# Optimization experiments

Measured on AMD Instinct MI355X. Metric: run time of the kernel, lower is better.

## Reference

```python
import jax, jax.numpy as jnp
import numpy as np

B = 4096        # batch
N_IN = 4096     # flattened input size
C = 128         # number of cores
A = 64          # axons (inputs) per core
O = 64          # neurons (outputs) per core
N_OUT = 1024    # number of output sources
CYCLES = 4      # ChipLatency
POOL_W = N_IN + 2 + C * O  # x cols | off(zero) | always_on(one) | core buffers


def setup_inputs() -> dict:
    key = jax.random.key(0)
    k1, k2, k3, k4 = jax.random.split(key, 4)
    x = jax.random.normal(k1, (B, N_IN), dtype=jnp.float32)
    # core_params[c] has shape (neurons_out, axons_in) = (O, A)
    W = jax.random.normal(k2, (C, O, A), dtype=jnp.float32) * 0.05
    # flat source index per (core, axon): encodes (is_input / is_off / is_always_on / buffer[core][neuron])
    axon_idx = jax.random.randint(k3, (C, A), 0, POOL_W, dtype=jnp.int32)
    out_idx = jax.random.randint(k4, (N_OUT,), 0, POOL_W, dtype=jnp.int32)
    return {"x": x, "W": W, "axon_idx": axon_idx, "out_idx": out_idx, "cycles": CYCLES}


def reference(x, W, axon_idx, out_idx, cycles):
    b = x.shape[0]
    c, o, a = W.shape
    zero_col = jnp.zeros((b, 1), x.dtype)   # is_off sources
    one_col = jnp.ones((b, 1), x.dtype)     # is_always_on sources
    buffers = jnp.zeros((b, c * o), x.dtype)  # all core buffers, flattened core-major

    def make_pool(buf):
        return jnp.concatenate([x, zero_col, one_col, buf], axis=1)  # (b, POOL_W)

    for _ in range(cycles):
        pool = make_pool(buffers)
        inp = pool[:, axon_idx]  # (b, c, a) fused get_signal_tensor gather
        # buffer[c] = relu(input_signals[c] @ core_matrix[c]) == relu(W[c] @ inp[c].T).T
        buffers = jax.nn.relu(jnp.einsum('coa,bca->bco', W, inp)).reshape(b, c * o)

    pool = make_pool(buffers)
    return pool[:, out_idx]  # (b, N_OUT) output_sources gather
```

## Files before the change

### kernel.cpp

```cpp
#include <hip/hip_runtime.h>

typedef __attribute__((ext_vector_type(8))) short short8;
typedef __attribute__((ext_vector_type(8))) __bf16 bf16x8;
typedef __attribute__((ext_vector_type(4))) float f32x4;
typedef __attribute__((ext_vector_type(4))) unsigned short ushort4_t;
typedef __attribute__((ext_vector_type(4))) unsigned int uint4_t;

#define NB   4096
#define NIN  4096
#define NX   4098
#define NC   128
#define NO   64
#define NA   64
#define NOUT 1024

__device__ __forceinline__ unsigned short f2bf(float f) {
  unsigned b = __builtin_bit_cast(unsigned, f);
  b += 0x7FFFu + ((b >> 16) & 1u);
  return (unsigned short)(b >> 16);
}
__device__ __forceinline__ float bf2f(unsigned short u) {
  return __builtin_bit_cast(float, (unsigned)u << 16);
}

__global__ __launch_bounds__(256) void prep_kernel(
    const float* __restrict__ x, const float* __restrict__ W,
    unsigned short* __restrict__ xT, unsigned short* __restrict__ Wb) {
  int bid = blockIdx.x, t = threadIdx.x;
  if (bid < 4096) {
    __shared__ unsigned short tile[64][68];
    int b0 = (bid >> 6) << 6, n0 = (bid & 63) << 6;
    int r = t >> 4, c4 = (t & 15) << 2;
#pragma unroll
    for (int rr = 0; rr < 4; ++rr) {
      int row = r + rr * 16;
      float4 v = *(const float4*)(x + (size_t)(b0 + row) * NIN + n0 + c4);
      tile[row][c4 + 0] = f2bf(v.x);
      tile[row][c4 + 1] = f2bf(v.y);
      tile[row][c4 + 2] = f2bf(v.z);
      tile[row][c4 + 3] = f2bf(v.w);
    }
    __syncthreads();
#pragma unroll
    for (int rr = 0; rr < 4; ++rr) {
      int nl = r + rr * 16;
      ushort4_t o;
      o.x = tile[c4 + 0][nl];
      o.y = tile[c4 + 1][nl];
      o.z = tile[c4 + 2][nl];
      o.w = tile[c4 + 3][nl];
      *(ushort4_t*)(xT + (size_t)(n0 + nl) * NB + b0 + c4) = o;
    }
  } else if (bid < 4096 + 256) {
    size_t i0 = (size_t)(bid - 4096) * 2048 + (size_t)t * 8;
    float4 v0 = *(const float4*)(W + i0);
    float4 v1 = *(const float4*)(W + i0 + 4);
    ushort4_t a, b;
    a.x = f2bf(v0.x); a.y = f2bf(v0.y); a.z = f2bf(v0.z); a.w = f2bf(v0.w);
    b.x = f2bf(v1.x); b.y = f2bf(v1.y); b.z = f2bf(v1.z); b.w = f2bf(v1.w);
    *(ushort4_t*)(Wb + i0) = a;
    *(ushort4_t*)(Wb + i0 + 4) = b;
  } else {
    int e = (bid - 4352) * 1024 + t * 4;
    int row = e >> 12, col = e & 4095;
    unsigned short val = (row == 0) ? (unsigned short)0 : (unsigned short)0x3F80;
    ushort4_t o = {val, val, val, val};
    *(ushort4_t*)(xT + (size_t)(NIN + row) * NB + col) = o;
  }
}

__global__ __launch_bounds__(1024) void mask_kernel(
    const int* __restrict__ oidx, unsigned char* __restrict__ mask) {
  int t = threadIdx.x;
#pragma unroll
  for (int i = t; i < NC * NO; i += 1024) mask[i] = 0;
  __syncthreads();
  if (t < NOUT) {
    int idx = oidx[t];
    if (idx >= NX) mask[idx - NX] = 1;
  }
}

template <int MODE>
__global__ __launch_bounds__(256) void cycle_kernel(
    const unsigned short* __restrict__ xT, const unsigned short* __restrict__ Wb,
    const unsigned short* __restrict__ bufPrev, unsigned short* __restrict__ bufNext,
    const int* __restrict__ axon, const unsigned char* __restrict__ mask,
    int first) {
  __shared__ __align__(16) unsigned short SM[64 * 264];
  int c = blockIdx.y;
  int t = threadIdx.x;
  int b0 = blockIdx.x << 8;
  const int* arow = axon + (c << 6);

  {
    int ao = t >> 5, bo = t & 31;
    const int* ar = arow + ao * 8;
    uint4_t rows[8];
#pragma unroll
    for (int r = 0; r < 8; ++r) {
      int idx = ar[r];
      const unsigned short* s = nullptr;
      if (idx < NX)      s = xT + (size_t)idx * NB;
      else if (!first)   s = bufPrev + (size_t)(idx - NX) * NB;
      if (s) rows[r] = *(const uint4_t*)(s + b0 + bo * 8);
      else   rows[r] = (uint4_t)(0u);
    }
    unsigned lo[4][4], hi[4][4];
#pragma unroll
    for (int p = 0; p < 4; ++p)
#pragma unroll
      for (int k = 0; k < 4; ++k) {
        unsigned wi = rows[2 * p][k], wj = rows[2 * p + 1][k];
        lo[p][k] = __builtin_amdgcn_perm(wj, wi, 0x05040100u);
        hi[p][k] = __builtin_amdgcn_perm(wj, wi, 0x07060302u);
      }
#pragma unroll
    for (int e = 0; e < 8; ++e) {
      int k = e >> 1;
      uint4_t col;
      if (e & 1) { col[0] = hi[0][k]; col[1] = hi[1][k]; col[2] = hi[2][k]; col[3] = hi[3][k]; }
      else       { col[0] = lo[0][k]; col[1] = lo[1][k]; col[2] = lo[2][k]; col[3] = lo[3][k]; }
      int b = bo * 8 + e;
      int sw = ao ^ (b & 7) ^ ((b >> 5) & 7);
      *(uint4_t*)&SM[b * 64 + (sw << 3)] = col;
    }
  }
  __syncthreads();

  int lane = t & 63, w = t >> 6;
  int ln = lane & 15, g = lane >> 4;
  const unsigned short* wrow = Wb + ((size_t)c << 12);

  f32x4 acc[4][4];
#pragma unroll
  for (int i = 0; i < 4; ++i)
#pragma unroll
    for (int j = 0; j < 4; ++j) acc[i][j] = (f32x4)(0.f);

#pragma unroll
  for (int ks = 0; ks < 2; ++ks) {
    short8 bw[4];
#pragma unroll
    for (int j = 0; j < 4; ++j)
      bw[j] = *(const short8*)(wrow + ((size_t)(j * 16 + ln) << 6) + ks * 32 + g * 8);

    short8 ag[4];
#pragma unroll
    for (int i = 0; i < 4; ++i) {
      int bl = (w << 6) + (i << 4) + ln;
      int c8 = (ks << 2) + g;
      int sw = c8 ^ (bl & 7) ^ ((bl >> 5) & 7);
      ag[i] = *(const short8*)&SM[bl * 64 + (sw << 3)];
    }

#pragma unroll
    for (int i = 0; i < 4; ++i)
#pragma unroll
      for (int j = 0; j < 4; ++j)
        acc[i][j] = __builtin_amdgcn_mfma_f32_16x16x32_bf16(
            __builtin_bit_cast(bf16x8, ag[i]), __builtin_bit_cast(bf16x8, bw[j]),
            acc[i][j], 0, 0, 0);
  }

  __syncthreads();
#pragma unroll
  for (int j = 0; j < 4; ++j) {
    int o = j * 16 + ln;
#pragma unroll
    for (int i = 0; i < 4; ++i) {
      ushort4_t pk;
#pragma unroll
      for (int r = 0; r < 4; ++r) pk[r] = f2bf(fmaxf(acc[i][j][r], 0.f));
      *(ushort4_t*)&SM[o * 264 + (w << 6) + (i << 4) + (g << 2)] = pk;
    }
  }
  __syncthreads();
#pragma unroll
  for (int it = 0; it < 16; ++it) {
    int row = it * 4 + w;
    if (MODE == 1 && mask[(c << 6) + row] == 0) continue;
    ushort4_t v = *(const ushort4_t*)&SM[row * 264 + (lane << 2)];
    *(ushort4_t*)(bufNext + ((size_t)((c << 6) + row)) * NB + b0 + (lane << 2)) = v;
  }
}

__global__ __launch_bounds__(256) void final_kernel(
    const unsigned short* __restrict__ xT, const unsigned short* __restrict__ bufFin,
    const int* __restrict__ out_idx, float* __restrict__ out) {
  __shared__ unsigned short tile[256][66];
  int j0 = blockIdx.x << 6, b0 = blockIdx.y << 8;
  int t = threadIdx.x;
  {
    int jl = t >> 2, bq = t & 3;
    int idx = out_idx[j0 + jl];
    const unsigned short* src = (idx < NX) ? xT + (size_t)idx * NB
                                           : bufFin + (size_t)(idx - NX) * NB;
    int jcol = jl ^ (bq << 4);
#pragma unroll
    for (int k = 0; k < 8; ++k) {
      short8 v = *(const short8*)(src + b0 + bq * 64 + k * 8);
#pragma unroll
      for (int m = 0; m < 8; ++m)
        tile[bq * 64 + k * 8 + m][jcol] = (unsigned short)v[m];
    }
  }
  __syncthreads();
  {
    int j = t & 63, ws = t >> 6;
#pragma unroll
    for (int bb = 0; bb < 64; ++bb) {
      int b = bb * 4 + ws;
      int jc = j ^ ((b >> 6) << 4);
      out[(size_t)(b0 + b) * NOUT + j0 + j] = bf2f(tile[b][jc]);
    }
  }
}

extern "C" void kernel_launch(void* const* d_in, const int* in_sizes, int n_in,
                              void* d_out, int out_size, void* d_ws, size_t ws_size,
                              hipStream_t stream) {
  const float* x    = (const float*)d_in[0];
  const float* W    = (const float*)d_in[1];
  const int*   axon = (const int*)d_in[2];
  const int*   oidx = (const int*)d_in[3];
  float* out = (float*)d_out;

  const size_t XT_BYTES  = (size_t)NX * NB * 2;
  const size_t WB_BYTES  = (size_t)NC * NO * NA * 2;
  const size_t BUF_BYTES = (size_t)NC * NO * NB * 2;
  const size_t MASK_B    = 8192;
  if (ws_size < XT_BYTES + WB_BYTES + 2 * BUF_BYTES + MASK_B) return;

  char* ws = (char*)d_ws;
  unsigned short* xT   = (unsigned short*)ws;
  unsigned short* Wb   = (unsigned short*)(ws + XT_BYTES);
  unsigned short* bufA = (unsigned short*)(ws + XT_BYTES + WB_BYTES);
  unsigned short* bufB = (unsigned short*)(ws + XT_BYTES + WB_BYTES + BUF_BYTES);
  unsigned char*  mask = (unsigned char*)(ws + XT_BYTES + WB_BYTES + 2 * BUF_BYTES);

  prep_kernel<<<4360, 256, 0, stream>>>(x, W, xT, Wb);
  mask_kernel<<<1, 1024, 0, stream>>>(oidx, mask);
  dim3 cg(NB / 256, NC);
  cycle_kernel<0><<<cg, 256, 0, stream>>>(xT, Wb, bufB, bufA, axon, mask, 1);
  cycle_kernel<0><<<cg, 256, 0, stream>>>(xT, Wb, bufA, bufB, axon, mask, 0);
  cycle_kernel<0><<<cg, 256, 0, stream>>>(xT, Wb, bufB, bufA, axon, mask, 0);
  cycle_kernel<1><<<cg, 256, 0, stream>>>(xT, Wb, bufA, bufB, axon, mask, 0);
  final_kernel<<<dim3(NOUT / 64, NB / 256), 256, 0, stream>>>(xT, bufB, oidx, out);
}
```

Measured before the change: 155.8 us.

## Skip buffer writes for unreferenced neurons and widen cycle blocks to 512 batch rows

A second mask is built from the axon indices, so the intermediate cycles only write buffer rows that some later axon actually reads. The output mask is kept for the last cycle. In that last cycle, whole 16-neuron groups with no referenced neuron also skip their weight loads and MFMAs. The cycle kernel now handles 512 batch rows per block with 512 threads and writes 16-byte stores, which halves the grid and doubles the LDS per block. The intent is to cut write bandwidth and wasted matrix work, at the cost of lower occupancy per CU.

```diff
diff --git a/kernel.cpp b/kernel.cpp
--- a/kernel.cpp
+++ b/kernel.cpp
@@ -70,31 +70,38 @@
 }
 
 __global__ __launch_bounds__(1024) void mask_kernel(
-    const int* __restrict__ oidx, unsigned char* __restrict__ mask) {
+    const int* __restrict__ axon, const int* __restrict__ oidx,
+    unsigned char* __restrict__ gmask, unsigned char* __restrict__ omask) {
   int t = threadIdx.x;
-#pragma unroll
-  for (int i = t; i < NC * NO; i += 1024) mask[i] = 0;
-  __syncthreads();
+  for (int i = t; i < NC * NO; i += 1024) { gmask[i] = 0; omask[i] = 0; }
+  __syncthreads();
+  for (int i = t; i < NC * NA; i += 1024) {
+    int idx = axon[i];
+    if (idx >= NX) gmask[idx - NX] = 1;
+  }
   if (t < NOUT) {
     int idx = oidx[t];
-    if (idx >= NX) mask[idx - NX] = 1;
+    if (idx >= NX) omask[idx - NX] = 1;
   }
 }
 
 template <int MODE>
-__global__ __launch_bounds__(256) void cycle_kernel(
+__global__ __launch_bounds__(512) void cycle_kernel(
     const unsigned short* __restrict__ xT, const unsigned short* __restrict__ Wb,
     const unsigned short* __restrict__ bufPrev, unsigned short* __restrict__ bufNext,
     const int* __restrict__ axon, const unsigned char* __restrict__ mask,
     int first) {
-  __shared__ __align__(16) unsigned short SM[64 * 264];
+  __shared__ __align__(16) unsigned short SM[64 * 520];
   int c = blockIdx.y;
   int t = threadIdx.x;
-  int b0 = blockIdx.x << 8;
+  int b0 = blockIdx.x << 9;
   const int* arow = axon + (c << 6);
 
+  int lane = t & 63, w = t >> 6;
+  int ln = lane & 15, g = lane >> 4;
+
   {
-    int ao = t >> 5, bo = t & 31;
+    int ao = w, bo = lane;
     const int* ar = arow + ao * 8;
     uint4_t rows[8];
 #pragma unroll
@@ -128,10 +135,15 @@
   }
   __syncthreads();
 
-  int lane = t & 63, w = t >> 6;
-  int ln = lane & 15, g = lane >> 4;
   const unsigned short* wrow = Wb + ((size_t)c << 12);
 
+  bool grp[4];
+#pragma unroll
+  for (int j = 0; j < 4; ++j) {
+    if (MODE == 1) grp[j] = __any((int)(mask[(c << 6) + j * 16 + ln] != 0));
+    else           grp[j] = true;
+  }
+
   f32x4 acc[4][4];
 #pragma unroll
   for (int i = 0; i < 4; ++i)
@@ -140,11 +152,6 @@
 
 #pragma unroll
   for (int ks = 0; ks < 2; ++ks) {
-    short8 bw[4];
-#pragma unroll
-    for (int j = 0; j < 4; ++j)
-      bw[j] = *(const short8*)(wrow + ((size_t)(j * 16 + ln) << 6) + ks * 32 + g * 8);
-
     short8 ag[4];
 #pragma unroll
     for (int i = 0; i < 4; ++i) {
@@ -153,14 +160,16 @@
       int sw = c8 ^ (bl & 7) ^ ((bl >> 5) & 7);
       ag[i] = *(const short8*)&SM[bl * 64 + (sw << 3)];
     }
-
-#pragma unroll
-    for (int i = 0; i < 4; ++i)
-#pragma unroll
-      for (int j = 0; j < 4; ++j)
+#pragma unroll
+    for (int j = 0; j < 4; ++j) {
+      if (!grp[j]) continue;
+      short8 bw = *(const short8*)(wrow + ((size_t)(j * 16 + ln) << 6) + ks * 32 + g * 8);
+#pragma unroll
+      for (int i = 0; i < 4; ++i)
         acc[i][j] = __builtin_amdgcn_mfma_f32_16x16x32_bf16(
-            __builtin_bit_cast(bf16x8, ag[i]), __builtin_bit_cast(bf16x8, bw[j]),
+            __builtin_bit_cast(bf16x8, ag[i]), __builtin_bit_cast(bf16x8, bw),
             acc[i][j], 0, 0, 0);
+    }
   }
 
   __syncthreads();
@@ -172,16 +181,16 @@
       ushort4_t pk;
 #pragma unroll
       for (int r = 0; r < 4; ++r) pk[r] = f2bf(fmaxf(acc[i][j][r], 0.f));
-      *(ushort4_t*)&SM[o * 264 + (w << 6) + (i << 4) + (g << 2)] = pk;
-    }
-  }
-  __syncthreads();
-#pragma unroll
-  for (int it = 0; it < 16; ++it) {
-    int row = it * 4 + w;
-    if (MODE == 1 && mask[(c << 6) + row] == 0) continue;
-    ushort4_t v = *(const ushort4_t*)&SM[row * 264 + (lane << 2)];
-    *(ushort4_t*)(bufNext + ((size_t)((c << 6) + row)) * NB + b0 + (lane << 2)) = v;
+      *(ushort4_t*)&SM[o * 520 + (w << 6) + (i << 4) + (g << 2)] = pk;
+    }
+  }
+  __syncthreads();
+#pragma unroll
+  for (int it = 0; it < 8; ++it) {
+    int row = it * 8 + w;
+    if (mask[(c << 6) + row] == 0) continue;
+    uint4_t v = *(const uint4_t*)&SM[row * 520 + (lane << 3)];
+    *(uint4_t*)(bufNext + ((size_t)((c << 6) + row)) * NB + b0 + (lane << 3)) = v;
   }
 }
 
@@ -230,21 +239,22 @@
   const size_t WB_BYTES  = (size_t)NC * NO * NA * 2;
   const size_t BUF_BYTES = (size_t)NC * NO * NB * 2;
   const size_t MASK_B    = 8192;
-  if (ws_size < XT_BYTES + WB_BYTES + 2 * BUF_BYTES + MASK_B) return;
+  if (ws_size < XT_BYTES + WB_BYTES + 2 * BUF_BYTES + 2 * MASK_B) return;
 
   char* ws = (char*)d_ws;
-  unsigned short* xT   = (unsigned short*)ws;
-  unsigned short* Wb   = (unsigned short*)(ws + XT_BYTES);
-  unsigned short* bufA = (unsigned short*)(ws + XT_BYTES + WB_BYTES);
-  unsigned short* bufB = (unsigned short*)(ws + XT_BYTES + WB_BYTES + BUF_BYTES);
-  unsigned char*  mask = (unsigned char*)(ws + XT_BYTES + WB_BYTES + 2 * BUF_BYTES);
+  unsigned short* xT    = (unsigned short*)ws;
+  unsigned short* Wb    = (unsigned short*)(ws + XT_BYTES);
+  unsigned short* bufA  = (unsigned short*)(ws + XT_BYTES + WB_BYTES);
+  unsigned short* bufB  = (unsigned short*)(ws + XT_BYTES + WB_BYTES + BUF_BYTES);
+  unsigned char*  gmask = (unsigned char*)(ws + XT_BYTES + WB_BYTES + 2 * BUF_BYTES);
+  unsigned char*  omask = gmask + MASK_B;
 
   prep_kernel<<<4360, 256, 0, stream>>>(x, W, xT, Wb);
-  mask_kernel<<<1, 1024, 0, stream>>>(oidx, mask);
-  dim3 cg(NB / 256, NC);
-  cycle_kernel<0><<<cg, 256, 0, stream>>>(xT, Wb, bufB, bufA, axon, mask, 1);
-  cycle_kernel<0><<<cg, 256, 0, stream>>>(xT, Wb, bufA, bufB, axon, mask, 0);
-  cycle_kernel<0><<<cg, 256, 0, stream>>>(xT, Wb, bufB, bufA, axon, mask, 0);
-  cycle_kernel<1><<<cg, 256, 0, stream>>>(xT, Wb, bufA, bufB, axon, mask, 0);
+  mask_kernel<<<1, 1024, 0, stream>>>(axon, oidx, gmask, omask);
+  dim3 cg(NB / 512, NC);
+  cycle_kernel<0><<<cg, 512, 0, stream>>>(xT, Wb, bufB, bufA, axon, gmask, 1);
+  cycle_kernel<0><<<cg, 512, 0, stream>>>(xT, Wb, bufA, bufB, axon, gmask, 0);
+  cycle_kernel<0><<<cg, 512, 0, stream>>>(xT, Wb, bufB, bufA, axon, gmask, 0);
+  cycle_kernel<1><<<cg, 512, 0, stream>>>(xT, Wb, bufA, bufB, axon, omask, 0);
   final_kernel<<<dim3(NOUT / 64, NB / 256), 256, 0, stream>>>(xT, bufB, oidx, out);
 }
```

After: 139.7 us. 10.3% less time.
